# Kernel optimization log

Measured on AMD Instinct MI355X. Metric: run time of the kernel, lower is better.

Reference implementation:

```python
import jax, jax.numpy as jnp
import numpy as np

K_SIZE = 3
STRIDE = 1
DIL = 1
PAD = (K_SIZE - 1) // 2 * DIL          # padding of the deformable conv
OFF_PAD = (K_SIZE - 1) // 2            # padding of the offset conv
KK = K_SIZE * K_SIZE


def setup_inputs() -> dict:
    key = jax.random.key(0)
    k1, k2, k3, k4 = jax.random.split(key, 4)
    B, C, H, W = 4, 256, 64, 64
    O = 256
    x = jax.random.normal(k1, (B, C, H, W), jnp.float32)
    # offset/mask conv params (small so sampled offsets stay in a realistic range)
    w_off = jax.random.normal(k2, (3 * KK, C, K_SIZE, K_SIZE), jnp.float32) * 0.01
    b_off = jax.random.normal(k3, (3 * KK,), jnp.float32) * 0.01
    # deformable conv weight (conv_dcn has bias=False in the source)
    w_dcn = jax.random.normal(k4, (O, C, K_SIZE, K_SIZE), jnp.float32) * (1.0 / np.sqrt(C * KK))
    return {"x": x, "w_off": w_off, "b_off": b_off, "w_dcn": w_dcn}


def _bilinear_sample(x, ys, xs):
    """x: [B,C,H,W]; ys, xs: [B,KK,Ho,Wo] fractional coords. Zero outside bounds.
    Returns [B,C,KK,Ho,Wo]."""
    B, C, H, W = x.shape
    _, K, Ho, Wo = ys.shape
    y0 = jnp.floor(ys)
    x0 = jnp.floor(xs)
    y1, x1 = y0 + 1.0, x0 + 1.0
    wy1 = ys - y0
    wy0 = 1.0 - wy1
    wx1 = xs - x0
    wx0 = 1.0 - wx1
    x_flat = x.reshape(B, C, H * W)

    def gather_term(yi, xi, wt):
        valid = (yi >= 0) & (yi < H) & (xi >= 0) & (xi < W)
        yc = jnp.clip(yi, 0, H - 1).astype(jnp.int32)
        xc = jnp.clip(xi, 0, W - 1).astype(jnp.int32)
        idx = (yc * W + xc).reshape(B, -1)                      # [B, K*Ho*Wo]
        g = jax.vmap(lambda xf, i: xf[:, i])(x_flat, idx)       # [B, C, K*Ho*Wo]
        w = (wt * valid.astype(wt.dtype)).reshape(B, 1, -1)
        return g * w

    out = (gather_term(y0, x0, wy0 * wx0)
           + gather_term(y0, x1, wy0 * wx1)
           + gather_term(y1, x0, wy1 * wx0)
           + gather_term(y1, x1, wy1 * wx1))
    return out.reshape(B, C, K, Ho, Wo)


def _dcn_v2(x, w_off, b_off, w_dcn):
    B, C, H, W = x.shape
    # offset/mask conv (standard conv, padding (k-1)//2)
    om = jax.lax.conv_general_dilated(
        x, w_off, (STRIDE, STRIDE), [(OFF_PAD, OFF_PAD)] * 2,
        dimension_numbers=("NCHW", "OIHW", "NCHW")) + b_off[None, :, None, None]
    offset = om[:, :2 * KK]                 # [B, 2*KK, Ho, Wo] as (dy0,dx0,dy1,dx1,...)
    mask = jax.nn.sigmoid(om[:, 2 * KK:])   # [B, KK, Ho, Wo]
    Ho, Wo = offset.shape[2], offset.shape[3]

    off = offset.reshape(B, KK, 2, Ho, Wo)
    off_y, off_x = off[:, :, 0], off[:, :, 1]

    kh = (jnp.arange(KK) // K_SIZE).astype(jnp.float32)
    kw = (jnp.arange(KK) % K_SIZE).astype(jnp.float32)
    py = (jnp.arange(Ho) * STRIDE - PAD).astype(jnp.float32)
    px = (jnp.arange(Wo) * STRIDE - PAD).astype(jnp.float32)

    ys = py[None, None, :, None] + (kh * DIL)[None, :, None, None] + off_y
    xs = px[None, None, None, :] + (kw * DIL)[None, :, None, None] + off_x

    sampled = _bilinear_sample(x, ys, xs)           # [B,C,KK,Ho,Wo]
    sampled = sampled * mask[:, None]               # modulated (DCNv2)
    w = w_dcn.reshape(w_dcn.shape[0], C, KK)
    return jnp.einsum("bckhw,ock->bohw", sampled, w)


def reference(x, w_off, b_off, w_dcn):
    return _dcn_v2(x, w_off, b_off, w_dcn)
```

## Files before the change

### kernel.cpp

```cpp
#include <hip/hip_runtime.h>

typedef __attribute__((ext_vector_type(8))) short short8;
typedef __attribute__((ext_vector_type(4))) float f32x4;
typedef __attribute__((ext_vector_type(16))) float f32x16;

#define CIN 256
#define OUTC 256
#define HWW 4096
#define IMG_H 64
#define IMG_W 64
#define SROW 264

__device__ __forceinline__ short f2bf(float f) {
    unsigned u = __float_as_uint(f);
    u += 0x7fffu + ((u >> 16) & 1u);
    return (short)(u >> 16);
}
__device__ __forceinline__ float bf2f(short s) {
    return __uint_as_float(((unsigned)(unsigned short)s) << 16);
}

__global__ __launch_bounds__(256) void prep(const float* __restrict__ x,
                                            const float* __restrict__ w_dcn,
                                            const float* __restrict__ w_off,
                                            short* __restrict__ xT,
                                            short* __restrict__ wF,
                                            short* __restrict__ wFo) {
    int bid = blockIdx.x;
    if (bid < 1024) {
        __shared__ float T[64][65];
        int p0 = (bid & 63) * 64;
        int c0 = ((bid >> 6) & 3) * 64;
        int b  = bid >> 8;
        int j = threadIdx.x & 63, i = threadIdx.x >> 6;
        const float* xb = x + ((size_t)b * CIN + c0) * HWW + p0;
#pragma unroll
        for (int k = 0; k < 16; ++k) {
            int row = i * 16 + k;
            T[row][j] = xb[(size_t)row * HWW + j];
        }
        __syncthreads();
        short* xTb = xT + ((size_t)b * HWW + p0) * CIN + c0;
#pragma unroll
        for (int k = 0; k < 16; ++k) {
            int prow = i * 16 + k;
            xTb[(size_t)prow * CIN + j] = f2bf(T[j][prow]);
        }
    } else if (bid < 1312) {
        int g = (bid - 1024) * 256 + threadIdx.x;
        int lane = g & 63;
        int rest = g >> 6;
        int og = rest & 7;
        int kidx = rest >> 3;
        int kp = kidx >> 4, kc = kidx & 15;
        int oc = og * 32 + (lane & 31);
        int cbase = kc * 16 + (lane >> 5) * 8;
        short8 v;
#pragma unroll
        for (int j = 0; j < 8; ++j)
            v[j] = f2bf(w_dcn[oc * 2304 + (cbase + j) * 9 + kp]);
        *(short8*)(wF + (size_t)g * 8) = v;
    } else {
        int g = (bid - 1312) * 256 + threadIdx.x;
        int lane = g & 63;
        int rest = g >> 6;
        int octile = rest & 1;
        int step = rest >> 1;
        int kp = step >> 3, chv = step & 7;
        int oc = octile * 16 + (lane & 15);
        int cbase = chv * 32 + (lane >> 4) * 8;
        short8 v;
#pragma unroll
        for (int j = 0; j < 8; ++j)
            v[j] = (oc < 27) ? f2bf(w_off[(oc * 256 + cbase + j) * 9 + kp]) : (short)0;
        *(short8*)(wFo + (size_t)g * 8) = v;
    }
}

__global__ __launch_bounds__(256) void offs_mfma(
        const short* __restrict__ xT, const short* __restrict__ wFo,
        float* __restrict__ P) {
    __shared__ short Sm[2][32 * SROW];

    int tid = threadIdx.x;
    int d = blockIdx.x;
    int L = (d & 7) * 64 + (d >> 3);
    int b = L >> 7;
    int ph = L & 127;
    int pbase = ph * 32;
    int prow = ph >> 1;
    int pc0 = (ph & 1) * 32;
    const short* xTb = xT + (size_t)b * HWW * CIN;

    int lane = tid & 63, wave = tid >> 6;
    int fr = lane & 15, fq = lane >> 4;
    int octile = wave & 1, pxt = wave >> 1;

    short8 st[4];

    auto loads = [&](int kp) {
        int yy = prow - 1 + kp / 3;
        int dx = kp % 3 - 1;
#pragma unroll
        for (int it = 0; it < 4; ++it) {
            int item = tid + it * 256;
            int cg8 = item & 31, px = item >> 5;
            int xx = pc0 + px + dx;
            bool ok = (yy >= 0 && yy < IMG_H && xx >= 0 && xx < IMG_W);
            int idx = ok ? ((yy * IMG_W + xx) * CIN + cg8 * 8) : 0;
            short8 v = *(const short8*)&xTb[idx];
            if (!ok) v = (short8){0,0,0,0,0,0,0,0};
            st[it] = v;
        }
    };
    auto writes = [&](int bufi) {
#pragma unroll
        for (int it = 0; it < 4; ++it) {
            int item = tid + it * 256;
            int cg8 = item & 31, px = item >> 5;
            *(short8*)&Sm[bufi][px * SROW + cg8 * 8] = st[it];
        }
    };

    f32x4 acc = (f32x4){0.f, 0.f, 0.f, 0.f};

    loads(0); writes(0);
    __syncthreads();
    for (int kp = 0; kp < 9; ++kp) {
        short8 aF[8];
#pragma unroll
        for (int chv = 0; chv < 8; ++chv)
            aF[chv] = *(const short8*)(wFo +
                    (((size_t)((kp * 8 + chv) * 2 + octile)) * 64 + lane) * 8);
        if (kp < 8) loads(kp + 1);
        const short* SmB = Sm[kp & 1];
#pragma unroll
        for (int chv = 0; chv < 8; ++chv) {
            short8 bF = *(const short8*)&SmB[(pxt * 16 + fr) * SROW + chv * 32 + fq * 8];
            acc = __builtin_amdgcn_mfma_f32_16x16x32_bf16(aF[chv], bF, acc, 0, 0, 0);
        }
        if (kp < 8) writes((kp + 1) & 1);
        __syncthreads();
    }

#pragma unroll
    for (int r = 0; r < 4; ++r) {
        int oc = octile * 16 + fq * 4 + r;
        if (oc < 27)
            P[((size_t)b * 32 + oc) * HWW + pbase + pxt * 16 + fr] = acc[r];
    }
}

__global__ __launch_bounds__(1024) void dcn_main(
        const short* __restrict__ xT, const float* __restrict__ b_off,
        const float* __restrict__ P, const short* __restrict__ wF,
        float* __restrict__ out) {
    __shared__ short Sm[2][64 * 256];
    __shared__ float4  preW[576];
    __shared__ ushort4 preI[576];

    int tid = threadIdx.x;
    int d = blockIdx.x;
    int L = (d & 7) * 32 + (d >> 3);
    int b = L >> 6;
    int row = L & 63;
    int pbase = row * 64;
    const short* xTb = xT + (size_t)b * HWW * CIN;

    if (tid < 576) {
        int e = tid;
        int px = e & 63, kp = e >> 6;
        int p = pbase + px;
        float oy = P[((size_t)b * 32 + 2 * kp) * HWW + p] + b_off[2 * kp];
        float ox = P[((size_t)b * 32 + 2 * kp + 1) * HWW + p] + b_off[2 * kp + 1];
        float ml = P[((size_t)b * 32 + 18 + kp) * HWW + p] + b_off[18 + kp];
        float m = 1.0f / (1.0f + expf(-ml));
        float ys = (float)(row - 1 + kp / 3) + oy;
        float xs = (float)(px - 1 + kp % 3) + ox;
        float y0f = floorf(ys), x0f = floorf(xs);
        float fy = ys - y0f, fx = xs - x0f;
        int iy0 = (int)y0f, ix0 = (int)x0f;
        int iy1 = iy0 + 1, ix1 = ix0 + 1;
        float vy0 = (iy0 >= 0 && iy0 < IMG_H) ? 1.f : 0.f;
        float vy1 = (iy1 >= 0 && iy1 < IMG_H) ? 1.f : 0.f;
        float vx0 = (ix0 >= 0 && ix0 < IMG_W) ? 1.f : 0.f;
        float vx1 = (ix1 >= 0 && ix1 < IMG_W) ? 1.f : 0.f;
        int ry0 = min(max(iy0, 0), IMG_H - 1) * IMG_W;
        int ry1 = min(max(iy1, 0), IMG_H - 1) * IMG_W;
        int cx0 = min(max(ix0, 0), IMG_W - 1);
        int cx1 = min(max(ix1, 0), IMG_W - 1);
        float wy0 = 1.f - fy, wy1 = fy, wx0 = 1.f - fx, wx1 = fx;
        preW[e] = make_float4(wy0 * wx0 * vy0 * vx0 * m, wy0 * wx1 * vy0 * vx1 * m,
                              wy1 * wx0 * vy1 * vx0 * m, wy1 * wx1 * vy1 * vx1 * m);
        preI[e] = make_ushort4((unsigned short)(ry0 + cx0), (unsigned short)(ry0 + cx1),
                               (unsigned short)(ry1 + cx0), (unsigned short)(ry1 + cx1));
    }
    __syncthreads();

    int lane = tid & 63, wave = tid >> 6;
    int og = wave & 7, kh = wave >> 3;
    int pxl = lane & 31, hl = lane >> 5, sw = lane & 15;

    int i_cg8 = tid & 31, i_px = tid >> 5;

    short8 st[2][4];

    auto loads = [&](int kp) {
#pragma unroll
        for (int it = 0; it < 2; ++it) {
            int px = i_px + it * 32;
            ushort4 iv = preI[kp * 64 + px];
            int co = i_cg8 * 8;
            st[it][0] = *(const short8*)&xTb[(int)iv.x * CIN + co];
            st[it][1] = *(const short8*)&xTb[(int)iv.y * CIN + co];
            st[it][2] = *(const short8*)&xTb[(int)iv.z * CIN + co];
            st[it][3] = *(const short8*)&xTb[(int)iv.w * CIN + co];
        }
    };
    auto writes = [&](int kp, int bufi) {
#pragma unroll
        for (int it = 0; it < 2; ++it) {
            int px = i_px + it * 32;
            float4 wv = preW[kp * 64 + px];
            short8 o;
#pragma unroll
            for (int j = 0; j < 8; ++j) {
                float v = wv.x * bf2f(st[it][0][j]) + wv.y * bf2f(st[it][1][j]) +
                          wv.z * bf2f(st[it][2][j]) + wv.w * bf2f(st[it][3][j]);
                o[j] = f2bf(v);
            }
            *(short8*)&Sm[bufi][px * 256 + ((i_cg8 ^ (px & 15)) * 8)] = o;
        }
    };

    f32x16 acc[2];
#pragma unroll
    for (int n = 0; n < 2; ++n)
#pragma unroll
        for (int r = 0; r < 16; ++r)
            acc[n][r] = 0.f;

    loads(0); writes(0, 0);
    __syncthreads();
    for (int kp = 0; kp < 9; ++kp) {
        short8 aF[8];
#pragma unroll
        for (int kc = 0; kc < 8; ++kc)
            aF[kc] = *(const short8*)(wF +
                    (((size_t)((kp * 16 + kh * 8 + kc) * 8 + og)) * 64 + lane) * 8);
        if (kp < 8) loads(kp + 1);
        const short* SmB = Sm[kp & 1];
#pragma unroll
        for (int kc = 0; kc < 8; ++kc) {
            int chunkb = (kh * 8 + kc) * 2 + hl;
#pragma unroll
            for (int n = 0; n < 2; ++n) {
                int px = n * 32 + pxl;
                short8 bF = *(const short8*)&SmB[px * 256 + ((chunkb ^ sw) * 8)];
                acc[n] = __builtin_amdgcn_mfma_f32_32x32x16_bf16(aF[kc], bF, acc[n], 0, 0, 0);
            }
        }
        if (kp < 8) writes(kp + 1, (kp + 1) & 1);
        __syncthreads();
    }

    float* SmF = (float*)Sm;
    if (kh == 1) {
#pragma unroll
        for (int n = 0; n < 2; ++n)
#pragma unroll
            for (int r = 0; r < 16; ++r) {
                int ocr = (r & 3) + 8 * (r >> 2) + 4 * hl;
                SmF[og * 2048 + ocr * 64 + n * 32 + pxl] = acc[n][r];
            }
    }
    __syncthreads();
    if (kh == 0) {
        float* outb = out + (size_t)b * (OUTC * HWW) + (size_t)og * 32 * HWW + pbase;
#pragma unroll
        for (int n = 0; n < 2; ++n)
#pragma unroll
            for (int r = 0; r < 16; ++r) {
                int ocr = (r & 3) + 8 * (r >> 2) + 4 * hl;
                float v = acc[n][r] + SmF[og * 2048 + ocr * 64 + n * 32 + pxl];
                outb[(size_t)ocr * HWW + n * 32 + pxl] = v;
            }
    }
}

extern "C" void kernel_launch(void* const* d_in, const int* in_sizes, int n_in,
                              void* d_out, int out_size, void* d_ws, size_t ws_size,
                              hipStream_t stream) {
    const float* x     = (const float*)d_in[0];
    const float* w_off = (const float*)d_in[1];
    const float* b_off = (const float*)d_in[2];
    const float* w_dcn = (const float*)d_in[3];
    float* out = (float*)d_out;

    short* xT  = (short*)d_ws;
    float* P   = (float*)(xT + (size_t)4 * HWW * CIN);
    short* wF  = (short*)(P + (size_t)4 * 32 * HWW);
    short* wFo = wF + (size_t)73728 * 8;

    prep<<<1348, 256, 0, stream>>>(x, w_dcn, w_off, xT, wF, wFo);
    offs_mfma<<<512, 256, 0, stream>>>(xT, wFo, P);
    dcn_main<<<256, 1024, 0, stream>>>(xT, b_off, P, wF, out);
}
```

Baseline: 62.26 us.

## Split dcn_main into half-row tiles with 512-thread blocks and no K-split reduction

Changes dcn_main from 256 blocks of 1024 threads, each covering a 64-pixel row with a two-way channel split reduced through shared memory, to 512 blocks of 512 threads, each covering 32 pixels with every wave accumulating all 256 input channels for 32 output channels. This removes the cross-wave reduction and its extra barrier, halves shared memory per block, and lets more blocks run per CU (launch_bounds 512,4) to improve occupancy and latency hiding. It also adopts a new swizzled LDS layout and wraps the MFMA loops in s_setprio. The cost is that each wave now loads both halves of the weight fragments per tap, and each block repeats the per-tap weight loads over half as many pixels.

Measured after the change: 107.5 us. 72.6% more time.

```diff
diff --git a/kernel.cpp b/kernel.cpp
--- a/kernel.cpp
+++ b/kernel.cpp
@@ -151,32 +151,34 @@
     }
 }
 
-__global__ __launch_bounds__(1024) void dcn_main(
+__global__ __launch_bounds__(512, 4) void dcn_main(
         const short* __restrict__ xT, const float* __restrict__ b_off,
         const float* __restrict__ P, const short* __restrict__ wF,
         float* __restrict__ out) {
-    __shared__ short Sm[2][64 * 256];
-    __shared__ float4  preW[576];
-    __shared__ ushort4 preI[576];
+    __shared__ short Sm[2][1024 * 8];
+    __shared__ float4  preW[288];
+    __shared__ ushort4 preI[288];
 
     int tid = threadIdx.x;
     int d = blockIdx.x;
-    int L = (d & 7) * 32 + (d >> 3);
-    int b = L >> 6;
-    int row = L & 63;
-    int pbase = row * 64;
+    int L = (d & 7) * 64 + (d >> 3);
+    int b = L >> 7;
+    int ph = L & 127;
+    int pbase = ph * 32;
+    int prow = ph >> 1;
+    int pc0 = (ph & 1) * 32;
     const short* xTb = xT + (size_t)b * HWW * CIN;
 
-    if (tid < 576) {
+    if (tid < 288) {
         int e = tid;
-        int px = e & 63, kp = e >> 6;
+        int px = e & 31, kp = e >> 5;
         int p = pbase + px;
         float oy = P[((size_t)b * 32 + 2 * kp) * HWW + p] + b_off[2 * kp];
         float ox = P[((size_t)b * 32 + 2 * kp + 1) * HWW + p] + b_off[2 * kp + 1];
         float ml = P[((size_t)b * 32 + 18 + kp) * HWW + p] + b_off[18 + kp];
         float m = 1.0f / (1.0f + expf(-ml));
-        float ys = (float)(row - 1 + kp / 3) + oy;
-        float xs = (float)(px - 1 + kp % 3) + ox;
+        float ys = (float)(prow - 1 + kp / 3) + oy;
+        float xs = (float)(pc0 + px - 1 + kp % 3) + ox;
         float y0f = floorf(ys), x0f = floorf(xs);
         float fy = ys - y0f, fx = xs - x0f;
         int iy0 = (int)y0f, ix0 = (int)x0f;
@@ -198,19 +200,19 @@
     __syncthreads();
 
     int lane = tid & 63, wave = tid >> 6;
-    int og = wave & 7, kh = wave >> 3;
-    int pxl = lane & 31, hl = lane >> 5, sw = lane & 15;
-
-    int i_cg8 = tid & 31, i_px = tid >> 5;
+    int og = wave;
+    int pxl = lane & 31, hl = lane >> 5;
+
+    int i_chunk = tid & 31, i_px0 = tid >> 5;
 
     short8 st[2][4];
 
     auto loads = [&](int kp) {
 #pragma unroll
         for (int it = 0; it < 2; ++it) {
-            int px = i_px + it * 32;
-            ushort4 iv = preI[kp * 64 + px];
-            int co = i_cg8 * 8;
+            int px = i_px0 + it * 16;
+            ushort4 iv = preI[kp * 32 + px];
+            int co = i_chunk * 8;
             st[it][0] = *(const short8*)&xTb[(int)iv.x * CIN + co];
             st[it][1] = *(const short8*)&xTb[(int)iv.y * CIN + co];
             st[it][2] = *(const short8*)&xTb[(int)iv.z * CIN + co];
@@ -220,8 +222,8 @@
     auto writes = [&](int kp, int bufi) {
 #pragma unroll
         for (int it = 0; it < 2; ++it) {
-            int px = i_px + it * 32;
-            float4 wv = preW[kp * 64 + px];
+            int px = i_px0 + it * 16;
+            float4 wv = preW[kp * 32 + px];
             short8 o;
 #pragma unroll
             for (int j = 0; j < 8; ++j) {
@@ -229,16 +231,13 @@
                           wv.z * bf2f(st[it][2][j]) + wv.w * bf2f(st[it][3][j]);
                 o[j] = f2bf(v);
             }
-            *(short8*)&Sm[bufi][px * 256 + ((i_cg8 ^ (px & 15)) * 8)] = o;
+            *(short8*)&Sm[bufi][(i_chunk * 32 + (px ^ i_chunk)) * 8] = o;
         }
     };
 
-    f32x16 acc[2];
-#pragma unroll
-    for (int n = 0; n < 2; ++n)
-#pragma unroll
-        for (int r = 0; r < 16; ++r)
-            acc[n][r] = 0.f;
+    f32x16 acc;
+#pragma unroll
+    for (int r = 0; r < 16; ++r) acc[r] = 0.f;
 
     loads(0); writes(0, 0);
     __syncthreads();
@@ -247,44 +246,39 @@
 #pragma unroll
         for (int kc = 0; kc < 8; ++kc)
             aF[kc] = *(const short8*)(wF +
-                    (((size_t)((kp * 16 + kh * 8 + kc) * 8 + og)) * 64 + lane) * 8);
+                    (((size_t)((kp * 16 + kc) * 8 + og)) * 64 + lane) * 8);
         if (kp < 8) loads(kp + 1);
         const short* SmB = Sm[kp & 1];
+        __builtin_amdgcn_s_setprio(1);
 #pragma unroll
         for (int kc = 0; kc < 8; ++kc) {
-            int chunkb = (kh * 8 + kc) * 2 + hl;
-#pragma unroll
-            for (int n = 0; n < 2; ++n) {
-                int px = n * 32 + pxl;
-                short8 bF = *(const short8*)&SmB[px * 256 + ((chunkb ^ sw) * 8)];
-                acc[n] = __builtin_amdgcn_mfma_f32_32x32x16_bf16(aF[kc], bF, acc[n], 0, 0, 0);
-            }
-        }
+            int c0 = kc * 2 + hl;
+            short8 bF = *(const short8*)&SmB[(c0 * 32 + (pxl ^ c0)) * 8];
+            acc = __builtin_amdgcn_mfma_f32_32x32x16_bf16(aF[kc], bF, acc, 0, 0, 0);
+        }
+        __builtin_amdgcn_s_setprio(0);
+        short8 aG[8];
+#pragma unroll
+        for (int kc = 0; kc < 8; ++kc)
+            aG[kc] = *(const short8*)(wF +
+                    (((size_t)((kp * 16 + 8 + kc) * 8 + og)) * 64 + lane) * 8);
+        __builtin_amdgcn_s_setprio(1);
+#pragma unroll
+        for (int kc = 0; kc < 8; ++kc) {
+            int c0 = (8 + kc) * 2 + hl;
+            short8 bF = *(const short8*)&SmB[(c0 * 32 + (pxl ^ c0)) * 8];
+            acc = __builtin_amdgcn_mfma_f32_32x32x16_bf16(aG[kc], bF, acc, 0, 0, 0);
+        }
+        __builtin_amdgcn_s_setprio(0);
         if (kp < 8) writes(kp + 1, (kp + 1) & 1);
         __syncthreads();
     }
 
-    float* SmF = (float*)Sm;
-    if (kh == 1) {
-#pragma unroll
-        for (int n = 0; n < 2; ++n)
-#pragma unroll
-            for (int r = 0; r < 16; ++r) {
-                int ocr = (r & 3) + 8 * (r >> 2) + 4 * hl;
-                SmF[og * 2048 + ocr * 64 + n * 32 + pxl] = acc[n][r];
-            }
-    }
-    __syncthreads();
-    if (kh == 0) {
-        float* outb = out + (size_t)b * (OUTC * HWW) + (size_t)og * 32 * HWW + pbase;
-#pragma unroll
-        for (int n = 0; n < 2; ++n)
-#pragma unroll
-            for (int r = 0; r < 16; ++r) {
-                int ocr = (r & 3) + 8 * (r >> 2) + 4 * hl;
-                float v = acc[n][r] + SmF[og * 2048 + ocr * 64 + n * 32 + pxl];
-                outb[(size_t)ocr * HWW + n * 32 + pxl] = v;
-            }
+    float* outb = out + (size_t)b * (OUTC * HWW) + (size_t)og * 32 * HWW + pbase;
+#pragma unroll
+    for (int r = 0; r < 16; ++r) {
+        int ocr = (r & 3) + 8 * (r >> 2) + 4 * hl;
+        outb[(size_t)ocr * HWW + pxl] = acc[r];
     }
 }
 
@@ -304,5 +298,5 @@
 
     prep<<<1348, 256, 0, stream>>>(x, w_dcn, w_off, xT, wF, wFo);
     offs_mfma<<<512, 256, 0, stream>>>(xT, wFo, P);
-    dcn_main<<<256, 1024, 0, stream>>>(xT, b_off, P, wF, out);
-}
+    dcn_main<<<512, 512, 0, stream>>>(xT, b_off, P, wF, out);
+}
```
